# Kernel optimization log

Measured on AMD Instinct MI355X. Metric: run time of the kernel, lower is better.

The kernel has to match this reference:

```python
import jax, jax.numpy as jnp
import numpy as np

NEG_SLOPE = 0.2  # PyG GATConv default negative_slope


def gat_conv(x, W, b, a_src, a_dst, src, dst, N, H, C):
    """PyG-style GATConv (v1 attention), concat heads, self-loops already in (src,dst)."""
    h = (x @ W).reshape(N, H, C)                       # [N,H,C]
    al_src = jnp.sum(h * a_src, axis=-1)               # [N,H]
    al_dst = jnp.sum(h * a_dst, axis=-1)               # [N,H]
    e = jax.nn.leaky_relu(al_src[src] + al_dst[dst], NEG_SLOPE)  # [E,H]
    m = jax.ops.segment_max(e, dst, num_segments=N)    # segment softmax (stable)
    m = jnp.where(jnp.isfinite(m), m, 0.0)
    ex = jnp.exp(e - m[dst])
    denom = jax.ops.segment_sum(ex, dst, num_segments=N)
    alpha = ex / (denom[dst] + 1e-16)                  # [E,H]
    msg = h[src] * alpha[..., None]                    # [E,H,C]
    out = jax.ops.segment_sum(msg, dst, num_segments=N)  # [N,H,C]
    return out.reshape(N, H * C) + b


def setup_inputs() -> dict:
    key = jax.random.key(0)
    ks = jax.random.split(key, 16)
    N, E, IN, HID, HEADS, OUT, G = 50000, 600000, 128, 64, 4, 10, 64
    x = jax.random.normal(ks[0], (N, IN), dtype=jnp.float32)
    edge_index = jax.random.randint(ks[1], (2, E), 0, N, dtype=jnp.int32)
    batch = jnp.sort(jax.random.randint(ks[2], (N,), 0, G, dtype=jnp.int32))
    s = 0.1
    p = {
        'W1': jax.random.normal(ks[3], (IN, HEADS * HID)) * s,
        'b1': jnp.zeros((HEADS * HID,), jnp.float32),
        'asrc1': jax.random.normal(ks[4], (HEADS, HID)) * s,
        'adst1': jax.random.normal(ks[5], (HEADS, HID)) * s,
        'W2': jax.random.normal(ks[6], (HEADS * HID, HEADS * HID)) * s,
        'b2': jnp.zeros((HEADS * HID,), jnp.float32),
        'asrc2': jax.random.normal(ks[7], (HEADS, HID)) * s,
        'adst2': jax.random.normal(ks[8], (HEADS, HID)) * s,
        'W3': jax.random.normal(ks[9], (HEADS * HID, HID)) * s,
        'b3': jnp.zeros((HID,), jnp.float32),
        'asrc3': jax.random.normal(ks[10], (1, HID)) * s,
        'adst3': jax.random.normal(ks[11], (1, HID)) * s,
        'linW': jax.random.normal(ks[12], (HID, OUT)) * s,
        'linb': jnp.zeros((OUT,), jnp.float32),
    }
    return dict(x=x, edge_index=edge_index, batch=batch, **p)


def reference(x, edge_index, batch, W1, b1, asrc1, adst1, W2, b2, asrc2, adst2,
              W3, b3, asrc3, adst3, linW, linb):
    N = x.shape[0]
    G = 64  # number of graphs
    loops = jnp.arange(N, dtype=edge_index.dtype)
    src = jnp.concatenate([edge_index[0], loops])  # PyG adds self-loops by default
    dst = jnp.concatenate([edge_index[1], loops])
    # eval mode: dropout is identity
    h = jax.nn.elu(gat_conv(x, W1, b1, asrc1, adst1, src, dst, N, 4, 64))
    h = jax.nn.elu(gat_conv(h, W2, b2, asrc2, adst2, src, dst, N, 4, 64))
    h = jax.nn.elu(gat_conv(h, W3, b3, asrc3, adst3, src, dst, N, 1, 64))
    # global mean pool over graphs
    sums = jax.ops.segment_sum(h, batch, num_segments=G)            # [G,64]
    cnts = jax.ops.segment_sum(jnp.ones((N,), h.dtype), batch, num_segments=G)
    pooled = sums / jnp.maximum(cnts, 1.0)[:, None]
    return pooled @ linW + linb                                      # [G,10]
```

## Files before the change

### kernel.cpp

```cpp
#include <hip/hip_runtime.h>
#include <hip/hip_bf16.h>
#include <math.h>

#define NEG_SLOPE 0.2f

typedef short short8 __attribute__((ext_vector_type(8)));
typedef float f32x4 __attribute__((ext_vector_type(4)));
typedef unsigned int u32;
typedef unsigned short u16;

__device__ __forceinline__ float lrelu(float x){ return x > 0.f ? x : NEG_SLOPE * x; }
__device__ __forceinline__ float elu_f(float x){ return x > 0.f ? x : __expf(x) - 1.f; }
__device__ __forceinline__ u16 f2bf(float f){
  __hip_bfloat16 h = __float2bfloat16(f);
  return *(u16*)&h;
}

__global__ void prep_kernel(const float* __restrict__ x, u16* __restrict__ xb, int n4,
                            const float* __restrict__ W1, u16* __restrict__ w1t,
                            const float* __restrict__ W2, u16* __restrict__ w2t,
                            const float* __restrict__ W3, u16* __restrict__ w3t,
                            int* __restrict__ cursor, int N,
                            float* __restrict__ sums, int* __restrict__ cnts){
  int i = blockIdx.x * 256 + threadIdx.x;
  if (i < n4){
    float4 v = ((const float4*)x)[i];
    ushort4 o;
    o.x = f2bf(v.x); o.y = f2bf(v.y); o.z = f2bf(v.z); o.w = f2bf(v.w);
    ((ushort4*)xb)[i] = o;
    return;
  }
  int t = i - n4;
  if (t < 128 * 256){
    int k = t >> 8, m = t & 255;
    w1t[m * 128 + k] = f2bf(W1[t]);
    return;
  }
  t -= 128 * 256;
  if (t < 256 * 256){
    int k = t >> 8, m = t & 255;
    w2t[m * 256 + k] = f2bf(W2[t]);
    return;
  }
  t -= 256 * 256;
  if (t < 256 * 64){
    int k = t >> 6, m = t & 63;
    w3t[m * 256 + k] = f2bf(W3[t]);
    return;
  }
  t -= 256 * 64;
  if (t < N){ cursor[t] = 0; return; }
  t -= N;
  if (t < 64 * 64){ sums[t] = 0.f; return; }
  t -= 64 * 64;
  if (t < 64) cnts[t] = 0;
}

__global__ void ell_kernel(const int* __restrict__ src, const int* __restrict__ dst,
                           int E, int N, int* cursor, int* __restrict__ ell){
  int i = blockIdx.x * 256 + threadIdx.x;
  if (i < E + N){
    int s, d;
    if (i < E){ s = src[i]; d = dst[i]; }
    else      { s = i - E;  d = i - E;  }
    int pos = atomicAdd(&cursor[d], 1);
    if (pos < 64) ell[(size_t)d * 64 + pos] = s;
  }
}

template<int BN>
__global__ __launch_bounds__(256) void gemm_mfma(const u16* __restrict__ A,
                                                 const u16* __restrict__ Bt,
                                                 u16* __restrict__ C,
                                                 const float* __restrict__ asrc,
                                                 const float* __restrict__ adst,
                                                 float* __restrict__ als,
                                                 float* __restrict__ ald,
                                                 int N, int K, int M){
  constexpr int BM = 128;
  constexpr int MI = (BN == 128) ? 4 : 2;
  constexpr int SB = BN * 8 / 256;
  constexpr int HH = (BN == 128) ? 4 : 1;
  __shared__ short As[8][BM][8];
  __shared__ short Bs[8][BN][8];
  const int tid = threadIdx.x;
  const int w = tid >> 6, lane = tid & 63;
  const int quad = lane >> 4, l16 = lane & 15;
  const int row0 = blockIdx.y * BM, col0 = blockIdx.x * BN;
  const int wrow = (BN == 128) ? (w >> 1) * 64 : w * 32;
  const int wcol = (BN == 128) ? (w & 1) * 64 : 0;

  f32x4 acc[MI][4];
#pragma unroll
  for (int i = 0; i < MI; i++)
#pragma unroll
    for (int j = 0; j < 4; j++) acc[i][j] = (f32x4){0.f, 0.f, 0.f, 0.f};

  for (int k0 = 0; k0 < K; k0 += 64){
    __syncthreads();
#pragma unroll
    for (int q = 0; q < 4; q++){
      int lb = q * 256 + w * 64;
      int li = lb + lane;
      int c = li >> 7, r = li & 127;
      int grow = min(row0 + r, N - 1);
      const u16* gp = A + (size_t)grow * K + k0 + c * 8;
      __builtin_amdgcn_global_load_lds((const __attribute__((address_space(1))) void*)gp,
                                       (__attribute__((address_space(3))) void*)((char*)&As[0][0][0] + (size_t)lb * 16),
                                       16, 0, 0);
    }
#pragma unroll
    for (int q = 0; q < SB; q++){
      int lb = q * 256 + w * 64;
      int li = lb + lane;
      int c = li / BN, n = li % BN;
      const u16* gp = Bt + (size_t)(col0 + n) * K + k0 + c * 8;
      __builtin_amdgcn_global_load_lds((const __attribute__((address_space(1))) void*)gp,
                                       (__attribute__((address_space(3))) void*)((char*)&Bs[0][0][0] + (size_t)lb * 16),
                                       16, 0, 0);
    }
    __syncthreads();
#pragma unroll
    for (int ks = 0; ks < 2; ks++){
      short8 a[MI], b[4];
#pragma unroll
      for (int i = 0; i < MI; i++) a[i] = *(const short8*)&As[ks * 4 + quad][wrow + i * 16 + l16][0];
#pragma unroll
      for (int j = 0; j < 4; j++)  b[j] = *(const short8*)&Bs[ks * 4 + quad][wcol + j * 16 + l16][0];
#pragma unroll
      for (int i = 0; i < MI; i++)
#pragma unroll
        for (int j = 0; j < 4; j++)
          acc[i][j] = __builtin_amdgcn_mfma_f32_16x16x32_bf16(a[i], b[j], acc[i][j], 0, 0, 0);
    }
  }

  const int head = (col0 + wcol) >> 6;
  float avs[4], avd[4];
#pragma unroll
  for (int j = 0; j < 4; j++){
    int c = j * 16 + l16;
    avs[j] = asrc[head * 64 + c];
    avd[j] = adst[head * 64 + c];
  }

#pragma unroll
  for (int i = 0; i < MI; i++){
#pragma unroll
    for (int rr = 0; rr < 4; rr++){
      int row = row0 + wrow + i * 16 + quad * 4 + rr;
      float ps = acc[i][0][rr] * avs[0] + acc[i][1][rr] * avs[1]
               + acc[i][2][rr] * avs[2] + acc[i][3][rr] * avs[3];
      float pd = acc[i][0][rr] * avd[0] + acc[i][1][rr] * avd[1]
               + acc[i][2][rr] * avd[2] + acc[i][3][rr] * avd[3];
#pragma unroll
      for (int off = 8; off > 0; off >>= 1){
        ps += __shfl_xor(ps, off);
        pd += __shfl_xor(pd, off);
      }
      if (row < N){
#pragma unroll
        for (int j = 0; j < 4; j++)
          C[(size_t)row * M + col0 + wcol + j * 16 + l16] = f2bf(acc[i][j][rr]);
        if (l16 == 0){
          als[(size_t)row * HH + head] = ps;
          ald[(size_t)row * HH + head] = pd;
        }
      }
    }
  }
}

template<bool OBF>
__global__ __launch_bounds__(256) void agg4_kernel(const u16* __restrict__ hb,
    const float* __restrict__ als, const float* __restrict__ ald,
    const int* __restrict__ degv, const int* __restrict__ ell,
    const float* __restrict__ bias, void* __restrict__ outv, int N){
  __shared__ float lex[4][256];
  __shared__ int lu[4][64];
  int wslot = threadIdx.x >> 6;
  int node = (blockIdx.x * 256 + threadIdx.x) >> 6;
  int lane = threadIdx.x & 63;
  if (node >= N) return;
  int deg = degv[node];
  float4 t4 = *(const float4*)(ald + node * 4);
  const int hh = lane >> 4;

  bool v = lane < deg;
  int u_raw = ell[(size_t)node * 64 + lane];
  int u = v ? u_raw : 0;
  float4 s = *(const float4*)(als + (size_t)u * 4);
  float4 exv;
  exv.x = v ? __expf(lrelu(s.x + t4.x)) : 0.f;
  exv.y = v ? __expf(lrelu(s.y + t4.y)) : 0.f;
  exv.z = v ? __expf(lrelu(s.z + t4.z)) : 0.f;
  exv.w = v ? __expf(lrelu(s.w + t4.w)) : 0.f;
  *(float4*)&lex[wslot][lane * 4] = exv;
  lu[wslot][lane] = u;
  asm volatile("s_waitcnt lgkmcnt(0)" ::: "memory");

  float a0 = 0.f, a1 = 0.f, a2 = 0.f, a3 = 0.f, denom = 0.f;
  const u16* hbl = hb + lane * 4;
#pragma unroll 8
  for (int jj = 0; jj < deg; jj++){
    float ex = lex[wslot][jj * 4 + hh];
    int uu = lu[wslot][jj];
    uint2 t = *(const uint2*)(hbl + (size_t)uu * 256);
    denom += ex;
    a0 += ex * __uint_as_float((t.x & 0xffffu) << 16);
    a1 += ex * __uint_as_float(t.x & 0xffff0000u);
    a2 += ex * __uint_as_float((t.y & 0xffffu) << 16);
    a3 += ex * __uint_as_float(t.y & 0xffff0000u);
  }
  float inv = 1.f / (denom + 1e-16f);
  int ch = lane * 4;
  float o0 = elu_f(a0 * inv + bias[ch]);
  float o1 = elu_f(a1 * inv + bias[ch + 1]);
  float o2 = elu_f(a2 * inv + bias[ch + 2]);
  float o3 = elu_f(a3 * inv + bias[ch + 3]);
  if (OBF){
    uint2 o;
    o.x = (u32)f2bf(o0) | ((u32)f2bf(o1) << 16);
    o.y = (u32)f2bf(o2) | ((u32)f2bf(o3) << 16);
    ((uint2*)outv)[(size_t)node * 64 + lane] = o;
  } else {
    *(float4*)((float*)outv + (size_t)node * 256 + ch) = make_float4(o0, o1, o2, o3);
  }
}

__global__ __launch_bounds__(256) void agg1_kernel(const u16* __restrict__ hb,
    const float* __restrict__ als, const float* __restrict__ ald,
    const int* __restrict__ degv, const int* __restrict__ ell,
    const float* __restrict__ bias, float* __restrict__ out, int N){
  __shared__ float lex[4][72];
  __shared__ int lu[4][72];
  int wslot = threadIdx.x >> 6;
  int node = (blockIdx.x * 256 + threadIdx.x) >> 6;
  int lane = threadIdx.x & 63;
  if (node >= N) return;
  int deg = degv[node];
  float adv = ald[node];

  bool v = lane < deg;
  int u_raw = ell[(size_t)node * 64 + lane];
  int u = v ? u_raw : 0;
  lex[wslot][lane] = v ? __expf(lrelu(als[u] + adv)) : 0.f;
  lu[wslot][lane] = u;
  if (lane < 8){ lex[wslot][64 + lane] = 0.f; lu[wslot][64 + lane] = 0; }
  asm volatile("s_waitcnt lgkmcnt(0)" ::: "memory");

  int eo = lane >> 4;
  int chb = (lane & 15) * 4;
  float a0 = 0.f, a1 = 0.f, a2 = 0.f, a3 = 0.f, denom = 0.f;
#pragma unroll 4
  for (int j2 = 0; j2 < deg; j2 += 4){
    int jj = j2 + eo;
    float ex = lex[wslot][jj];
    int uu = lu[wslot][jj];
    uint2 t = *(const uint2*)(hb + (size_t)uu * 64 + chb);
    denom += ex;
    a0 += ex * __uint_as_float((t.x & 0xffffu) << 16);
    a1 += ex * __uint_as_float(t.x & 0xffff0000u);
    a2 += ex * __uint_as_float((t.y & 0xffffu) << 16);
    a3 += ex * __uint_as_float(t.y & 0xffff0000u);
  }
#pragma unroll
  for (int off = 16; off < 64; off <<= 1){
    denom += __shfl_xor(denom, off);
    a0 += __shfl_xor(a0, off); a1 += __shfl_xor(a1, off);
    a2 += __shfl_xor(a2, off); a3 += __shfl_xor(a3, off);
  }
  if (eo == 0){
    float inv = 1.f / (denom + 1e-16f);
    float o0 = elu_f(a0 * inv + bias[chb]);
    float o1 = elu_f(a1 * inv + bias[chb + 1]);
    float o2 = elu_f(a2 * inv + bias[chb + 2]);
    float o3 = elu_f(a3 * inv + bias[chb + 3]);
    *(float4*)(out + (size_t)node * 64 + chb) = make_float4(o0, o1, o2, o3);
  }
}

__global__ void pool_kernel(const float* __restrict__ f, const int* __restrict__ batch,
                            float* sums, int* cnts, int N){
  int lane = threadIdx.x;
  int s = blockIdx.x * 128;
  if (s >= N) return;
  int e = min(s + 128, N);
  float acc = 0.f;
  int cnt = 0;
  int cur = batch[s];
  for (int n = s; n < e; n++){
    int g = batch[n];
    if (g != cur){
      atomicAdd(&sums[cur * 64 + lane], acc);
      if (lane == 0) atomicAdd(&cnts[cur], cnt);
      acc = 0.f; cnt = 0; cur = g;
    }
    acc += f[(size_t)n * 64 + lane];
    cnt++;
  }
  atomicAdd(&sums[cur * 64 + lane], acc);
  if (lane == 0) atomicAdd(&cnts[cur], cnt);
}

__global__ void final_kernel(const float* __restrict__ sums, const int* __restrict__ cnts,
                             const float* __restrict__ linW, const float* __restrict__ linb,
                             float* __restrict__ out){
  int t = threadIdx.x;
  if (t >= 640) return;
  int g = t / 10, o = t % 10;
  float c = fmaxf((float)cnts[g], 1.f);
  float acc = 0.f;
#pragma unroll
  for (int k = 0; k < 64; k++) acc += sums[g * 64 + k] * linW[k * 10 + o];
  out[t] = acc / c + linb[o];
}

extern "C" void kernel_launch(void* const* d_in, const int* in_sizes, int n_in,
                              void* d_out, int out_size, void* d_ws, size_t ws_size,
                              hipStream_t stream) {
  const float* x     = (const float*)d_in[0];
  const int*   ei    = (const int*)  d_in[1];
  const int*   batch = (const int*)  d_in[2];
  const float* W1    = (const float*)d_in[3];
  const float* b1    = (const float*)d_in[4];
  const float* asrc1 = (const float*)d_in[5];
  const float* adst1 = (const float*)d_in[6];
  const float* W2    = (const float*)d_in[7];
  const float* b2    = (const float*)d_in[8];
  const float* asrc2 = (const float*)d_in[9];
  const float* adst2 = (const float*)d_in[10];
  const float* W3    = (const float*)d_in[11];
  const float* b3    = (const float*)d_in[12];
  const float* asrc3 = (const float*)d_in[13];
  const float* adst3 = (const float*)d_in[14];
  const float* linW  = (const float*)d_in[15];
  const float* linb  = (const float*)d_in[16];

  const int N = in_sizes[0] / 128;
  const int E = in_sizes[1] / 2;
  const int Etot = E + N;
  const int G = 64;
  const int* src = ei;
  const int* dst = ei + E;

  char* p = (char*)d_ws;
  auto carve = [&](size_t bytes) -> char* {
    char* r = p;
    p += (bytes + 255) & ~(size_t)255;
    return r;
  };
  u16*   xb       = (u16*)  carve((size_t)N * 128 * 2);
  u16*   w1t      = (u16*)  carve((size_t)256 * 128 * 2);
  u16*   w2t      = (u16*)  carve((size_t)256 * 256 * 2);
  u16*   w3t      = (u16*)  carve((size_t)64 * 256 * 2);
  u16*   hb       = (u16*)  carve((size_t)N * 256 * 2);
  u16*   featb    = (u16*)  carve((size_t)N * 256 * 2);
  float* out3     = (float*)carve((size_t)N * 64 * 4);
  float* als      = (float*)carve((size_t)N * 4 * 4);
  float* ald      = (float*)carve((size_t)N * 4 * 4);
  int*   cursor   = (int*)  carve((size_t)N * 4);
  int*   ell      = (int*)  carve((size_t)N * 64 * 4);
  float* sums     = (float*)carve((size_t)G * 64 * 4);
  int*   cnts     = (int*)  carve((size_t)G * 4);

  const int n4 = N * 128 / 4;
  const int prep_items = n4 + 128 * 256 + 256 * 256 + 256 * 64 + N + G * 64 + G;

  prep_kernel<<<(prep_items + 255) / 256, 256, 0, stream>>>(x, xb, n4, W1, w1t, W2, w2t, W3, w3t,
                                                            cursor, N, sums, cnts);

  ell_kernel<<<(Etot + 255) / 256, 256, 0, stream>>>(src, dst, E, N, cursor, ell);

  const int nby = (N + 127) / 128;
  const int wpn_grid = (N + 3) / 4;

  gemm_mfma<128><<<dim3(2, nby), 256, 0, stream>>>(xb, w1t, hb, asrc1, adst1, als, ald, N, 128, 256);
  agg4_kernel<true><<<wpn_grid, 256, 0, stream>>>(hb, als, ald, cursor, ell, b1, featb, N);

  gemm_mfma<128><<<dim3(2, nby), 256, 0, stream>>>(featb, w2t, hb, asrc2, adst2, als, ald, N, 256, 256);
  agg4_kernel<true><<<wpn_grid, 256, 0, stream>>>(hb, als, ald, cursor, ell, b2, featb, N);

  gemm_mfma<64><<<dim3(1, nby), 256, 0, stream>>>(featb, w3t, hb, asrc3, adst3, als, ald, N, 256, 64);
  agg1_kernel<<<wpn_grid, 256, 0, stream>>>(hb, als, ald, cursor, ell, b3, out3, N);

  pool_kernel<<<(N + 127) / 128, 64, 0, stream>>>(out3, batch, sums, cnts, N);
  final_kernel<<<1, 640, 0, stream>>>(sums, cnts, linW, linb, (float*)d_out);
}
```

Before: 365.6 us.

## Fuse ELL build into prep, drop GEMM LDS staging, widen aggregation loads

The separate ELL-construction kernel is folded into the prep kernel, and a single hipMemsetAsync zeroes the cursor, sums and counts, which removes one launch and the in-kernel zeroing. The MFMA GEMM no longer stages A and B tiles through LDS; each lane loads its bf16 fragments straight from global memory, which drops the barriers but relies on caches to absorb the redundant loads across waves. The aggregation kernels use 16-byte loads, with each lane covering 8 channels. In agg4 the two wave halves handle alternating edges and are combined with a cross-half shuffle; the LDS arrays are padded so that odd degrees read zeros.

```diff
diff --git a/kernel.cpp b/kernel.cpp
--- a/kernel.cpp
+++ b/kernel.cpp
@@ -11,6 +11,8 @@
 
 __device__ __forceinline__ float lrelu(float x){ return x > 0.f ? x : NEG_SLOPE * x; }
 __device__ __forceinline__ float elu_f(float x){ return x > 0.f ? x : __expf(x) - 1.f; }
+__device__ __forceinline__ float blo(u32 w){ return __uint_as_float(w << 16); }
+__device__ __forceinline__ float bhi(u32 w){ return __uint_as_float(w & 0xffff0000u); }
 __device__ __forceinline__ u16 f2bf(float f){
   __hip_bfloat16 h = __float2bfloat16(f);
   return *(u16*)&h;
@@ -20,8 +22,8 @@
                             const float* __restrict__ W1, u16* __restrict__ w1t,
                             const float* __restrict__ W2, u16* __restrict__ w2t,
                             const float* __restrict__ W3, u16* __restrict__ w3t,
-                            int* __restrict__ cursor, int N,
-                            float* __restrict__ sums, int* __restrict__ cnts){
+                            const int* __restrict__ src, const int* __restrict__ dst,
+                            int E, int N, int* cursor, int* __restrict__ ell){
   int i = blockIdx.x * 256 + threadIdx.x;
   if (i < n4){
     float4 v = ((const float4*)x)[i];
@@ -49,20 +51,10 @@
     return;
   }
   t -= 256 * 64;
-  if (t < N){ cursor[t] = 0; return; }
-  t -= N;
-  if (t < 64 * 64){ sums[t] = 0.f; return; }
-  t -= 64 * 64;
-  if (t < 64) cnts[t] = 0;
-}
-
-__global__ void ell_kernel(const int* __restrict__ src, const int* __restrict__ dst,
-                           int E, int N, int* cursor, int* __restrict__ ell){
-  int i = blockIdx.x * 256 + threadIdx.x;
-  if (i < E + N){
+  if (t < E + N){
     int s, d;
-    if (i < E){ s = src[i]; d = dst[i]; }
-    else      { s = i - E;  d = i - E;  }
+    if (t < E){ s = src[t]; d = dst[t]; }
+    else      { s = t - E;  d = t - E;  }
     int pos = atomicAdd(&cursor[d], 1);
     if (pos < 64) ell[(size_t)d * 64 + pos] = s;
   }
@@ -77,16 +69,12 @@
                                                  float* __restrict__ als,
                                                  float* __restrict__ ald,
                                                  int N, int K, int M){
-  constexpr int BM = 128;
   constexpr int MI = (BN == 128) ? 4 : 2;
-  constexpr int SB = BN * 8 / 256;
   constexpr int HH = (BN == 128) ? 4 : 1;
-  __shared__ short As[8][BM][8];
-  __shared__ short Bs[8][BN][8];
   const int tid = threadIdx.x;
   const int w = tid >> 6, lane = tid & 63;
   const int quad = lane >> 4, l16 = lane & 15;
-  const int row0 = blockIdx.y * BM, col0 = blockIdx.x * BN;
+  const int row0 = blockIdx.y * 128, col0 = blockIdx.x * BN;
   const int wrow = (BN == 128) ? (w >> 1) * 64 : w * 32;
   const int wcol = (BN == 128) ? (w & 1) * 64 : 0;
 
@@ -96,43 +84,29 @@
 #pragma unroll
     for (int j = 0; j < 4; j++) acc[i][j] = (f32x4){0.f, 0.f, 0.f, 0.f};
 
-  for (int k0 = 0; k0 < K; k0 += 64){
-    __syncthreads();
-#pragma unroll
-    for (int q = 0; q < 4; q++){
-      int lb = q * 256 + w * 64;
-      int li = lb + lane;
-      int c = li >> 7, r = li & 127;
-      int grow = min(row0 + r, N - 1);
-      const u16* gp = A + (size_t)grow * K + k0 + c * 8;
-      __builtin_amdgcn_global_load_lds((const __attribute__((address_space(1))) void*)gp,
-                                       (__attribute__((address_space(3))) void*)((char*)&As[0][0][0] + (size_t)lb * 16),
-                                       16, 0, 0);
-    }
-#pragma unroll
-    for (int q = 0; q < SB; q++){
-      int lb = q * 256 + w * 64;
-      int li = lb + lane;
-      int c = li / BN, n = li % BN;
-      const u16* gp = Bt + (size_t)(col0 + n) * K + k0 + c * 8;
-      __builtin_amdgcn_global_load_lds((const __attribute__((address_space(1))) void*)gp,
-                                       (__attribute__((address_space(3))) void*)((char*)&Bs[0][0][0] + (size_t)lb * 16),
-                                       16, 0, 0);
-    }
-    __syncthreads();
-#pragma unroll
-    for (int ks = 0; ks < 2; ks++){
-      short8 a[MI], b[4];
-#pragma unroll
-      for (int i = 0; i < MI; i++) a[i] = *(const short8*)&As[ks * 4 + quad][wrow + i * 16 + l16][0];
-#pragma unroll
-      for (int j = 0; j < 4; j++)  b[j] = *(const short8*)&Bs[ks * 4 + quad][wcol + j * 16 + l16][0];
-#pragma unroll
-      for (int i = 0; i < MI; i++)
-#pragma unroll
-        for (int j = 0; j < 4; j++)
-          acc[i][j] = __builtin_amdgcn_mfma_f32_16x16x32_bf16(a[i], b[j], acc[i][j], 0, 0, 0);
-    }
+  const u16* ap[MI];
+  const u16* bp[4];
+#pragma unroll
+  for (int i = 0; i < MI; i++){
+    int r = min(row0 + wrow + i * 16 + l16, N - 1);
+    ap[i] = A + (size_t)r * K + quad * 8;
+  }
+#pragma unroll
+  for (int j = 0; j < 4; j++)
+    bp[j] = Bt + (size_t)(col0 + wcol + j * 16 + l16) * K + quad * 8;
+
+#pragma unroll 2
+  for (int k0 = 0; k0 < K; k0 += 32){
+    short8 a[MI], b[4];
+#pragma unroll
+    for (int i = 0; i < MI; i++) a[i] = *(const short8*)(ap[i] + k0);
+#pragma unroll
+    for (int j = 0; j < 4; j++)  b[j] = *(const short8*)(bp[j] + k0);
+#pragma unroll
+    for (int i = 0; i < MI; i++)
+#pragma unroll
+      for (int j = 0; j < 4; j++)
+        acc[i][j] = __builtin_amdgcn_mfma_f32_16x16x32_bf16(a[i], b[j], acc[i][j], 0, 0, 0);
   }
 
   const int head = (col0 + wcol) >> 6;
@@ -171,24 +145,21 @@
   }
 }
 
-template<bool OBF>
 __global__ __launch_bounds__(256) void agg4_kernel(const u16* __restrict__ hb,
     const float* __restrict__ als, const float* __restrict__ ald,
     const int* __restrict__ degv, const int* __restrict__ ell,
-    const float* __restrict__ bias, void* __restrict__ outv, int N){
-  __shared__ float lex[4][256];
-  __shared__ int lu[4][64];
+    const float* __restrict__ bias, u16* __restrict__ out, int N){
+  __shared__ float lex[4][264];
+  __shared__ int lu[4][66];
   int wslot = threadIdx.x >> 6;
   int node = (blockIdx.x * 256 + threadIdx.x) >> 6;
   int lane = threadIdx.x & 63;
   if (node >= N) return;
   int deg = degv[node];
   float4 t4 = *(const float4*)(ald + node * 4);
-  const int hh = lane >> 4;
 
   bool v = lane < deg;
-  int u_raw = ell[(size_t)node * 64 + lane];
-  int u = v ? u_raw : 0;
+  int u = v ? ell[(size_t)node * 64 + lane] : 0;
   float4 s = *(const float4*)(als + (size_t)u * 4);
   float4 exv;
   exv.x = v ? __expf(lrelu(s.x + t4.x)) : 0.f;
@@ -197,34 +168,43 @@
   exv.w = v ? __expf(lrelu(s.w + t4.w)) : 0.f;
   *(float4*)&lex[wslot][lane * 4] = exv;
   lu[wslot][lane] = u;
+  if (lane < 8) lex[wslot][256 + lane] = 0.f;
+  if (lane == 8){ lu[wslot][64] = 0; lu[wslot][65] = 0; }
   asm volatile("s_waitcnt lgkmcnt(0)" ::: "memory");
 
-  float a0 = 0.f, a1 = 0.f, a2 = 0.f, a3 = 0.f, denom = 0.f;
-  const u16* hbl = hb + lane * 4;
-#pragma unroll 8
-  for (int jj = 0; jj < deg; jj++){
+  const int half = lane >> 5;
+  const int l32 = lane & 31;
+  const int hh = l32 >> 3;
+  const u16* hbl = hb + l32 * 8;
+  float a[8] = {0.f,0.f,0.f,0.f,0.f,0.f,0.f,0.f};
+  float denom = 0.f;
+#pragma unroll 4
+  for (int it = 0; it * 2 < deg; it++){
+    int jj = it * 2 + half;
     float ex = lex[wslot][jj * 4 + hh];
     int uu = lu[wslot][jj];
-    uint2 t = *(const uint2*)(hbl + (size_t)uu * 256);
+    uint4 t = *(const uint4*)(hbl + (size_t)uu * 256);
     denom += ex;
-    a0 += ex * __uint_as_float((t.x & 0xffffu) << 16);
-    a1 += ex * __uint_as_float(t.x & 0xffff0000u);
-    a2 += ex * __uint_as_float((t.y & 0xffffu) << 16);
-    a3 += ex * __uint_as_float(t.y & 0xffff0000u);
-  }
-  float inv = 1.f / (denom + 1e-16f);
-  int ch = lane * 4;
-  float o0 = elu_f(a0 * inv + bias[ch]);
-  float o1 = elu_f(a1 * inv + bias[ch + 1]);
-  float o2 = elu_f(a2 * inv + bias[ch + 2]);
-  float o3 = elu_f(a3 * inv + bias[ch + 3]);
-  if (OBF){
-    uint2 o;
-    o.x = (u32)f2bf(o0) | ((u32)f2bf(o1) << 16);
-    o.y = (u32)f2bf(o2) | ((u32)f2bf(o3) << 16);
-    ((uint2*)outv)[(size_t)node * 64 + lane] = o;
-  } else {
-    *(float4*)((float*)outv + (size_t)node * 256 + ch) = make_float4(o0, o1, o2, o3);
+    a[0] += ex * blo(t.x); a[1] += ex * bhi(t.x);
+    a[2] += ex * blo(t.y); a[3] += ex * bhi(t.y);
+    a[4] += ex * blo(t.z); a[5] += ex * bhi(t.z);
+    a[6] += ex * blo(t.w); a[7] += ex * bhi(t.w);
+  }
+  denom += __shfl_xor(denom, 32);
+#pragma unroll
+  for (int k = 0; k < 8; k++) a[k] += __shfl_xor(a[k], 32);
+  if (half == 0){
+    float inv = 1.f / (denom + 1e-16f);
+    int ch = l32 * 8;
+    float o[8];
+#pragma unroll
+    for (int k = 0; k < 8; k++) o[k] = elu_f(a[k] * inv + bias[ch + k]);
+    uint4 pk;
+    pk.x = (u32)f2bf(o[0]) | ((u32)f2bf(o[1]) << 16);
+    pk.y = (u32)f2bf(o[2]) | ((u32)f2bf(o[3]) << 16);
+    pk.z = (u32)f2bf(o[4]) | ((u32)f2bf(o[5]) << 16);
+    pk.w = (u32)f2bf(o[6]) | ((u32)f2bf(o[7]) << 16);
+    ((uint4*)(out + (size_t)node * 256))[l32] = pk;
   }
 }
 
@@ -242,41 +222,42 @@
   float adv = ald[node];
 
   bool v = lane < deg;
-  int u_raw = ell[(size_t)node * 64 + lane];
-  int u = v ? u_raw : 0;
+  int u = v ? ell[(size_t)node * 64 + lane] : 0;
   lex[wslot][lane] = v ? __expf(lrelu(als[u] + adv)) : 0.f;
   lu[wslot][lane] = u;
   if (lane < 8){ lex[wslot][64 + lane] = 0.f; lu[wslot][64 + lane] = 0; }
   asm volatile("s_waitcnt lgkmcnt(0)" ::: "memory");
 
-  int eo = lane >> 4;
-  int chb = (lane & 15) * 4;
-  float a0 = 0.f, a1 = 0.f, a2 = 0.f, a3 = 0.f, denom = 0.f;
-#pragma unroll 4
-  for (int j2 = 0; j2 < deg; j2 += 4){
+  int eo = lane >> 3;
+  int chb = (lane & 7) * 8;
+  float a[8] = {0.f,0.f,0.f,0.f,0.f,0.f,0.f,0.f};
+  float denom = 0.f;
+#pragma unroll 2
+  for (int j2 = 0; j2 < deg; j2 += 8){
     int jj = j2 + eo;
     float ex = lex[wslot][jj];
     int uu = lu[wslot][jj];
-    uint2 t = *(const uint2*)(hb + (size_t)uu * 64 + chb);
+    uint4 t = *(const uint4*)(hb + (size_t)uu * 64 + chb);
     denom += ex;
-    a0 += ex * __uint_as_float((t.x & 0xffffu) << 16);
-    a1 += ex * __uint_as_float(t.x & 0xffff0000u);
-    a2 += ex * __uint_as_float((t.y & 0xffffu) << 16);
-    a3 += ex * __uint_as_float(t.y & 0xffff0000u);
-  }
-#pragma unroll
-  for (int off = 16; off < 64; off <<= 1){
+    a[0] += ex * blo(t.x); a[1] += ex * bhi(t.x);
+    a[2] += ex * blo(t.y); a[3] += ex * bhi(t.y);
+    a[4] += ex * blo(t.z); a[5] += ex * bhi(t.z);
+    a[6] += ex * blo(t.w); a[7] += ex * bhi(t.w);
+  }
+#pragma unroll
+  for (int off = 8; off < 64; off <<= 1){
     denom += __shfl_xor(denom, off);
-    a0 += __shfl_xor(a0, off); a1 += __shfl_xor(a1, off);
-    a2 += __shfl_xor(a2, off); a3 += __shfl_xor(a3, off);
+#pragma unroll
+    for (int k = 0; k < 8; k++) a[k] += __shfl_xor(a[k], off);
   }
   if (eo == 0){
     float inv = 1.f / (denom + 1e-16f);
-    float o0 = elu_f(a0 * inv + bias[chb]);
-    float o1 = elu_f(a1 * inv + bias[chb + 1]);
-    float o2 = elu_f(a2 * inv + bias[chb + 2]);
-    float o3 = elu_f(a3 * inv + bias[chb + 3]);
-    *(float4*)(out + (size_t)node * 64 + chb) = make_float4(o0, o1, o2, o3);
+    float o[8];
+#pragma unroll
+    for (int k = 0; k < 8; k++) o[k] = elu_f(a[k] * inv + bias[chb + k]);
+    float* op = out + (size_t)node * 64 + chb;
+    *(float4*)op       = make_float4(o[0], o[1], o[2], o[3]);
+    *(float4*)(op + 4) = make_float4(o[4], o[5], o[6], o[7]);
   }
 }
 
@@ -359,27 +340,28 @@
   float* out3     = (float*)carve((size_t)N * 64 * 4);
   float* als      = (float*)carve((size_t)N * 4 * 4);
   float* ald      = (float*)carve((size_t)N * 4 * 4);
-  int*   cursor   = (int*)  carve((size_t)N * 4);
   int*   ell      = (int*)  carve((size_t)N * 64 * 4);
-  float* sums     = (float*)carve((size_t)G * 64 * 4);
-  int*   cnts     = (int*)  carve((size_t)G * 4);
+  size_t zbytes = (size_t)N * 4 + (size_t)G * 64 * 4 + (size_t)G * 4;
+  char*  zbase  = carve(zbytes);
+  int*   cursor = (int*)zbase;
+  float* sums   = (float*)(zbase + (size_t)N * 4);
+  int*   cnts   = (int*)(zbase + (size_t)N * 4 + (size_t)G * 64 * 4);
 
   const int n4 = N * 128 / 4;
-  const int prep_items = n4 + 128 * 256 + 256 * 256 + 256 * 64 + N + G * 64 + G;
-
+  const int prep_items = n4 + 128 * 256 + 256 * 256 + 256 * 64 + Etot;
+
+  hipMemsetAsync(zbase, 0, zbytes, stream);
   prep_kernel<<<(prep_items + 255) / 256, 256, 0, stream>>>(x, xb, n4, W1, w1t, W2, w2t, W3, w3t,
-                                                            cursor, N, sums, cnts);
-
-  ell_kernel<<<(Etot + 255) / 256, 256, 0, stream>>>(src, dst, E, N, cursor, ell);
+                                                            src, dst, E, N, cursor, ell);
 
   const int nby = (N + 127) / 128;
   const int wpn_grid = (N + 3) / 4;
 
   gemm_mfma<128><<<dim3(2, nby), 256, 0, stream>>>(xb, w1t, hb, asrc1, adst1, als, ald, N, 128, 256);
-  agg4_kernel<true><<<wpn_grid, 256, 0, stream>>>(hb, als, ald, cursor, ell, b1, featb, N);
+  agg4_kernel<<<wpn_grid, 256, 0, stream>>>(hb, als, ald, cursor, ell, b1, featb, N);
 
   gemm_mfma<128><<<dim3(2, nby), 256, 0, stream>>>(featb, w2t, hb, asrc2, adst2, als, ald, N, 256, 256);
-  agg4_kernel<true><<<wpn_grid, 256, 0, stream>>>(hb, als, ald, cursor, ell, b2, featb, N);
+  agg4_kernel<<<wpn_grid, 256, 0, stream>>>(hb, als, ald, cursor, ell, b2, featb, N);
 
   gemm_mfma<64><<<dim3(1, nby), 256, 0, stream>>>(featb, w3t, hb, asrc3, adst3, als, ald, N, 256, 64);
   agg1_kernel<<<wpn_grid, 256, 0, stream>>>(hb, als, ald, cursor, ell, b3, out3, N);
```

Result: slower. 397.4 us (+8.7%).
